# Kernel optimization log

Measured on AMD Instinct MI355X. Metric: run time of the kernel, lower is better.

Reference implementation:

```python
import jax, jax.numpy as jnp
import numpy as np

MARGIN = 0.1
LAMBDA_EFFECT = 0.5

B, T_V, K, T_S = 32, 8192, 64, 128


def setup_inputs() -> dict:
    key = jax.random.key(0)
    k1, k2, k3, k4, k5 = jax.random.split(key, 5)
    pred_orig = jax.random.normal(k1, (B, T_V), dtype=jnp.float32)
    pred_intervened = jax.random.normal(k2, (K, B, T_V), dtype=jnp.float32)
    intervened_indices = jax.random.randint(k3, (K,), 0, T_S, dtype=jnp.int32)
    # GT alignment mask: sparse-ish binary alignment between frames and sentences
    gt_mask = jax.random.bernoulli(k4, 0.2, (B, T_V, T_S)).astype(jnp.int32)
    # prefix-valid video mask: valid length per batch in [T_V//2, T_V]
    lengths = jax.random.randint(k5, (B,), T_V // 2, T_V + 1, dtype=jnp.int32)
    mask_video = (jnp.arange(T_V, dtype=jnp.int32)[None, :] < lengths[:, None]).astype(jnp.int32)
    return {
        "pred_orig": pred_orig,
        "pred_intervened": pred_intervened,
        "intervened_indices": intervened_indices,
        "gt_mask": gt_mask,
        "mask_video": mask_video,
    }


def reference(pred_orig, pred_intervened, intervened_indices, gt_mask, mask_video):
    # pred_orig: [B,T], pred_intervened: [K,B,T], gt_mask: [B,T,S], mask_video: [B,T]
    prob_orig = jax.nn.sigmoid(pred_orig)                 # [B,T]
    prob_int = jax.nn.sigmoid(pred_intervened)            # [K,B,T]
    effect = jnp.abs(prob_orig[None, :, :] - prob_int)    # [K,B,T]

    valid = mask_video.astype(bool)                       # [B,T] (prefix mask == :T_v_valid slice)
    # gather intervened sentence columns: [B,T,K] -> [K,B,T]
    gt_sel = jnp.transpose(gt_mask[:, :, intervened_indices], (2, 0, 1))

    aligned = (gt_sel > 0) & valid[None]                  # [K,B,T]
    non_aligned = (gt_sel == 0) & valid[None]             # [K,B,T]

    cnt_a = aligned.sum(axis=-1)                          # [K,B]
    cnt_n = non_aligned.sum(axis=-1)                      # [K,B]

    ea = jnp.sum(effect * aligned, axis=-1) / jnp.maximum(cnt_a, 1)
    en = jnp.sum(effect * non_aligned, axis=-1) / jnp.maximum(cnt_n, 1)

    per_pair = jnp.where((cnt_a > 0) & (cnt_n > 0),
                         jax.nn.relu(MARGIN - (ea - en)),
                         jnp.zeros_like(ea))
    num_interventions = pred_orig.shape[0] * pred_intervened.shape[0]
    alignment_consistency = per_pair.sum() / max(num_interventions, 1)
    total_intervention_loss = alignment_consistency * LAMBDA_EFFECT
    return alignment_consistency, total_intervention_loss
```

## Files before the change

### kernel.cpp

```cpp
#include <hip/hip_runtime.h>
#include <cstdint>

#define BB 32
#define TV 8192
#define KK 64
#define TS 128
#define MARGIN_F 0.1f
#define LAMBDA_F 0.5f

typedef unsigned long long u64;
typedef unsigned int u32;

static constexpr int KB_PAIRS = KK * BB;
static constexpr int W32_PER_B = TV / 32;
static constexpr int W64_PER_B = TV / 64;


__global__ __launch_bounds__(64) void plane_kernel(
    const int* __restrict__ gt, const int* __restrict__ mv,
    u32* __restrict__ vbit, u32* __restrict__ pl,
    int* __restrict__ len, int* __restrict__ mw) {
  const int lane = threadIdx.x;
  const int blk = blockIdx.x;
  const int b = blk >> 8;
  const int g2 = blk & 255;
  const int grow = b * TV + g2 * 32;

  __shared__ __align__(16) int gtile[32 * TS];

  const int mvv = (lane < 32) ? mv[grow + lane] : 0;
  const u32 V32 = (u32)__ballot(mvv != 0);
  if (lane == 0) {
    vbit[b * W32_PER_B + g2] = V32;
    if (V32) {
      atomicAdd(&len[b], __popc(V32));
      atomicMax(&mw[b], g2);
    }
  }

  const int g64 = g2 >> 1, h = g2 & 1;
  u32* outp = pl + ((size_t)(b * 128 + g64) * TS) * 2 + h;

  if (V32 == 0u) {
    outp[2 * lane] = 0u;
    outp[2 * (lane + 64)] = 0u;
    return;
  }

  {
    const char* gsrc = (const char*)(gt + (size_t)grow * TS);
    char* ldst = (char*)gtile;
#pragma unroll
    for (int i = 0; i < 16; ++i) {
      __builtin_amdgcn_global_load_lds(
          (const __attribute__((address_space(1))) u32*)(gsrc + i * 1024 +
                                                         lane * 16),
          (__attribute__((address_space(3))) u32*)(ldst + i * 1024), 16, 0, 0);
    }
  }
  __syncthreads();

#pragma unroll
  for (int p = 0; p < 2; ++p) {
    const int s = lane + 64 * p;
    u32 wbits = 0;
#pragma unroll
    for (int r = 0; r < 32; ++r)
      if (gtile[r * TS + s] > 0) wbits |= 1u << r;
    outp[2 * s] = wbits & V32;
  }
}

__global__ __launch_bounds__(256, 4) void reduce_kernel(
    const float* __restrict__ po, const float* __restrict__ pi,
    const int* __restrict__ idx,
    const u32* __restrict__ vbit, const u32* __restrict__ pl,
    const int* __restrict__ mw,
    float* __restrict__ gsa, float* __restrict__ gsv,
    float* __restrict__ gca) {
  const int tid = threadIdx.x;
  const int lane = tid & 63;
  const int w = tid >> 6;
  const int kb = blockIdx.x;
  const int b = kb & (BB - 1);
  const int k = kb >> 5;
  const int c = idx[k];
  const u64* plb = (const u64*)pl + (size_t)b * (128 * TS) + c;
  const u64* vrow = (const u64*)vbit + (size_t)b * W64_PER_B;
  const float* pirow = pi + (size_t)kb * TV;
  const float* porow = po + (size_t)b * TV;

  __shared__ float rs[4][2];
  __shared__ int rca;
  if (tid == 0) rca = 0;
  __syncthreads();

  const int nch = min(8, (mw[b] + 32) >> 5);
  const int sh = (tid & 15) * 4;
  float sa = 0.f, sv = 0.f;
#pragma unroll 2
  for (int cc = 0; cc < nch; ++cc) {
    const int t = cc * 1024 + tid * 4;
    const int widx = t >> 6;
    const u64 vw = vrow[widx];
    const u32 vb4 = (u32)((vw >> sh) & 15ull);
    if (vb4) {
      const u64 aw = plb[(size_t)widx * TS] & vw;
      const u32 ab4 = (u32)((aw >> sh) & 15ull);
      const float4 x = *(const float4*)(pirow + t);
      const float4 p = *(const float4*)(porow + t);
      const float e0 =
          fabsf(__fdividef(1.f, 1.f + __expf(-p.x)) -
                __fdividef(1.f, 1.f + __expf(-x.x)));
      const float e1 =
          fabsf(__fdividef(1.f, 1.f + __expf(-p.y)) -
                __fdividef(1.f, 1.f + __expf(-x.y)));
      const float e2 =
          fabsf(__fdividef(1.f, 1.f + __expf(-p.z)) -
                __fdividef(1.f, 1.f + __expf(-x.z)));
      const float e3 =
          fabsf(__fdividef(1.f, 1.f + __expf(-p.w)) -
                __fdividef(1.f, 1.f + __expf(-x.w)));
      if (vb4 & 1u) sv += e0;
      if (vb4 & 2u) sv += e1;
      if (vb4 & 4u) sv += e2;
      if (vb4 & 8u) sv += e3;
      if (ab4 & 1u) sa += e0;
      if (ab4 & 2u) sa += e1;
      if (ab4 & 4u) sa += e2;
      if (ab4 & 8u) sa += e3;
    }
  }
#pragma unroll
  for (int off = 32; off; off >>= 1) {
    sa += __shfl_xor(sa, off);
    sv += __shfl_xor(sv, off);
  }
  if (lane == 0) {
    rs[w][0] = sa;
    rs[w][1] = sv;
  }
  if (tid < W64_PER_B)
    atomicAdd(&rca, __popcll(plb[(size_t)tid * TS] & vrow[tid]));
  __syncthreads();
  if (tid == 0) {
    gsa[kb] = rs[0][0] + rs[1][0] + rs[2][0] + rs[3][0];
    gsv[kb] = rs[0][1] + rs[1][1] + rs[2][1] + rs[3][1];
    gca[kb] = (float)rca;
  }
}

__global__ __launch_bounds__(256) void fin_kernel(
    const float* __restrict__ gsa, const float* __restrict__ gsv,
    const float* __restrict__ gca, const int* __restrict__ len,
    float* __restrict__ out) {
  float s = 0.f;
  for (int i = threadIdx.x; i < KB_PAIRS; i += 256) {
    const int b = i & (BB - 1);
    const float ca = gca[i];
    const float cn = (float)len[b] - ca;
    if (ca > 0.f && cn > 0.f) {
      const float sa = gsa[i];
      const float sv = gsv[i];
      const float d = MARGIN_F - (sa / ca - (sv - sa) / cn);
      s += d > 0.f ? d : 0.f;
    }
  }
#pragma unroll
  for (int off = 32; off > 0; off >>= 1) s += __shfl_down(s, off);
  __shared__ float ws4[4];
  if ((threadIdx.x & 63) == 0) ws4[threadIdx.x >> 6] = s;
  __syncthreads();
  if (threadIdx.x == 0) {
    const float S = ws4[0] + ws4[1] + ws4[2] + ws4[3];
    const float ac = S * (1.0f / (float)KB_PAIRS);
    out[0] = ac;
    out[1] = ac * LAMBDA_F;
  }
}

extern "C" void kernel_launch(void* const* d_in, const int* in_sizes, int n_in,
                              void* d_out, int out_size, void* d_ws, size_t ws_size,
                              hipStream_t stream) {
  const float* pred_orig = (const float*)d_in[0];
  const float* pred_int  = (const float*)d_in[1];
  const int*   idx       = (const int*)d_in[2];
  const int*   gt        = (const int*)d_in[3];
  const int*   mv        = (const int*)d_in[4];
  float* out = (float*)d_out;

  float* gsa = (float*)d_ws;
  float* gsv = gsa + KB_PAIRS;
  float* gca = gsv + KB_PAIRS;
  int*   len = (int*)(gca + KB_PAIRS);
  int*   mw  = len + BB;
  u32*   vbit = (u32*)(mw + BB);
  u32*   pl   = vbit + BB * W32_PER_B;

  hipMemsetAsync(len, 0, 2 * BB * sizeof(int), stream);
  plane_kernel<<<BB * W32_PER_B, 64, 0, stream>>>(gt, mv, vbit, pl, len, mw);
  reduce_kernel<<<KB_PAIRS, 256, 0, stream>>>(pred_orig, pred_int, idx, vbit,
                                              pl, mw, gsa, gsv, gca);
  fin_kernel<<<1, 256, 0, stream>>>(gsa, gsv, gca, len, out);
}
```

Before: 282.4 us.

## Double-buffer LDS DMA across four row groups per plane-kernel block

Each plane_kernel block now processes four consecutive 32-row groups instead of one, using two LDS buffers. The global-to-LDS load for the next group is issued before the bit-transpose of the current one, with explicit vmcnt waits and no block barrier. The aim is to hide load latency behind the transpose and cut per-block launch and mask-load overhead. In exchange, LDS per block doubles, which lowers how many waves can sit on each CU, and correctness now depends on hand-counted wait counts.

```diff
diff --git a/kernel.cpp b/kernel.cpp
--- a/kernel.cpp
+++ b/kernel.cpp
@@ -16,59 +16,100 @@
 static constexpr int W64_PER_B = TV / 64;
 
 
+__device__ __forceinline__ void dma16(const int* __restrict__ gsrc_i,
+                                      int* ldst_i, int lane) {
+  const char* gsrc = (const char*)gsrc_i;
+  char* ldst = (char*)ldst_i;
+#pragma unroll
+  for (int i = 0; i < 16; ++i) {
+    __builtin_amdgcn_global_load_lds(
+        (const __attribute__((address_space(1))) u32*)(gsrc + i * 1024 +
+                                                       lane * 16),
+        (__attribute__((address_space(3))) u32*)(ldst + i * 1024), 16, 0, 0);
+  }
+}
+
+__device__ __forceinline__ void trs(const int* bufp, u32 Vm,
+                                    u32* __restrict__ outp, int lane) {
+  if (Vm == 0u) {
+    outp[2 * lane] = 0u;
+    outp[2 * (lane + 64)] = 0u;
+    return;
+  }
+#pragma unroll
+  for (int p = 0; p < 2; ++p) {
+    const int s = lane + 64 * p;
+    u32 wb = 0;
+#pragma unroll
+    for (int r = 0; r < 32; ++r)
+      if (bufp[r * TS + s] > 0) wb |= 1u << r;
+    outp[2 * s] = wb & Vm;
+  }
+}
+
+#define WAITC(N)                                         \
+  asm volatile("s_waitcnt vmcnt(" #N ")" ::: "memory"); \
+  __builtin_amdgcn_sched_barrier(0)
+
 __global__ __launch_bounds__(64) void plane_kernel(
     const int* __restrict__ gt, const int* __restrict__ mv,
     u32* __restrict__ vbit, u32* __restrict__ pl,
     int* __restrict__ len, int* __restrict__ mw) {
   const int lane = threadIdx.x;
-  const int blk = blockIdx.x;
-  const int b = blk >> 8;
-  const int g2 = blk & 255;
-  const int grow = b * TV + g2 * 32;
-
-  __shared__ __align__(16) int gtile[32 * TS];
-
-  const int mvv = (lane < 32) ? mv[grow + lane] : 0;
-  const u32 V32 = (u32)__ballot(mvv != 0);
+  const int wid = blockIdx.x;
+  __shared__ __align__(16) int buf0[32 * TS];
+  __shared__ __align__(16) int buf1[32 * TS];
+
+  const int g0 = wid * 4;
+  const int rbase = g0 * 32;
+
+  const int m0 = mv[rbase + lane];
+  const int m1 = mv[rbase + 64 + lane];
+  const u64 B0 = __ballot(m0 != 0);
+  const u64 B1 = __ballot(m1 != 0);
+  u32 V[4];
+  V[0] = (u32)B0;
+  V[1] = (u32)(B0 >> 32);
+  V[2] = (u32)B1;
+  V[3] = (u32)(B1 >> 32);
+
   if (lane == 0) {
-    vbit[b * W32_PER_B + g2] = V32;
-    if (V32) {
-      atomicAdd(&len[b], __popc(V32));
-      atomicMax(&mw[b], g2);
+#pragma unroll
+    for (int j = 0; j < 4; ++j) {
+      const int g = g0 + j, b = g >> 8, g2 = g & 255;
+      vbit[b * W32_PER_B + g2] = V[j];
+      if (V[j]) {
+        atomicAdd(&len[b], __popc(V[j]));
+        atomicMax(&mw[b], g2);
+      }
     }
   }
 
-  const int g64 = g2 >> 1, h = g2 & 1;
-  u32* outp = pl + ((size_t)(b * 128 + g64) * TS) * 2 + h;
-
-  if (V32 == 0u) {
-    outp[2 * lane] = 0u;
-    outp[2 * (lane + 64)] = 0u;
-    return;
-  }
-
-  {
-    const char* gsrc = (const char*)(gt + (size_t)grow * TS);
-    char* ldst = (char*)gtile;
-#pragma unroll
-    for (int i = 0; i < 16; ++i) {
-      __builtin_amdgcn_global_load_lds(
-          (const __attribute__((address_space(1))) u32*)(gsrc + i * 1024 +
-                                                         lane * 16),
-          (__attribute__((address_space(3))) u32*)(ldst + i * 1024), 16, 0, 0);
-    }
-  }
-  __syncthreads();
-
-#pragma unroll
-  for (int p = 0; p < 2; ++p) {
-    const int s = lane + 64 * p;
-    u32 wbits = 0;
-#pragma unroll
-    for (int r = 0; r < 32; ++r)
-      if (gtile[r * TS + s] > 0) wbits |= 1u << r;
-    outp[2 * s] = wbits & V32;
-  }
+  u32* outp[4];
+#pragma unroll
+  for (int j = 0; j < 4; ++j) {
+    const int g = g0 + j, b = g >> 8, g2 = g & 255;
+    outp[j] = pl + ((size_t)(b * 128 + (g2 >> 1)) * TS) * 2 + (g2 & 1);
+  }
+
+  const int* gbase = gt + (size_t)rbase * TS;
+
+  if (V[0]) dma16(gbase, buf0, lane);
+  WAITC(0);
+
+  if (V[1]) dma16(gbase + 1 * 32 * TS, buf1, lane);
+  trs(buf0, V[0], outp[0], lane);
+  WAITC(2);
+
+  if (V[2]) dma16(gbase + 2 * 32 * TS, buf0, lane);
+  trs(buf1, V[1], outp[1], lane);
+  WAITC(2);
+
+  if (V[3]) dma16(gbase + 3 * 32 * TS, buf1, lane);
+  trs(buf0, V[2], outp[2], lane);
+  WAITC(2);
+
+  trs(buf1, V[3], outp[3], lane);
 }
 
 __global__ __launch_bounds__(256, 4) void reduce_kernel(
@@ -198,7 +239,7 @@
   u32*   pl   = vbit + BB * W32_PER_B;
 
   hipMemsetAsync(len, 0, 2 * BB * sizeof(int), stream);
-  plane_kernel<<<BB * W32_PER_B, 64, 0, stream>>>(gt, mv, vbit, pl, len, mw);
+  plane_kernel<<<2048, 64, 0, stream>>>(gt, mv, vbit, pl, len, mw);
   reduce_kernel<<<KB_PAIRS, 256, 0, stream>>>(pred_orig, pred_int, idx, vbit,
                                               pl, mw, gsa, gsv, gca);
   fin_kernel<<<1, 256, 0, stream>>>(gsa, gsv, gca, len, out);
```

New measurement: 293.7 us. 1.04x slower.
